# Performance work log

Hardware: AMD Instinct MI355X
Metric: run time of the kernel (lower is better)

## Reference

```python
import jax, jax.numpy as jnp
from jax import lax
import numpy as np

LOD = 60          # latent_obs_dim
LSD = 2 * LOD     # latent state dim
ACT = 10          # action dim
K = 15            # num_basis
BW = 3            # bandwidth
H_CTRL = 60       # control net hidden units
B, T = 1024, 150


def elup1(x):
    # elu(x) + 1, standard RKN positive-variance activation
    return jnp.where(x >= 0, x + 1.0, jnp.exp(x))


def setup_inputs() -> dict:
    key = jax.random.key(0)
    ks = jax.random.split(key, 14)
    inp = {
        "latent_obs": jax.random.normal(ks[0], (B, T, LOD), jnp.float32),
        "obs_vars": jax.random.uniform(ks[1], (B, T, LOD), jnp.float32) + 0.01,
        "action": jax.random.normal(ks[2], (B, T, ACT), jnp.float32),
        "initial_mean": jax.random.normal(ks[3], (B, LSD), jnp.float32),
        "initial_cov_u": jnp.ones((B, LOD), jnp.float32),
        "initial_cov_l": jnp.ones((B, LOD), jnp.float32),
        "initial_cov_s": jnp.zeros((B, LOD), jnp.float32),
        # transition model: K banded basis matrices per quadrant
        "tm11_basis": 0.05 * jax.random.normal(ks[4], (K, LOD, LOD), jnp.float32),
        "tm12_basis": 0.05 * jax.random.normal(ks[5], (K, LOD, LOD), jnp.float32),
        "tm21_basis": 0.05 * jax.random.normal(ks[6], (K, LOD, LOD), jnp.float32),
        "tm22_basis": 0.05 * jax.random.normal(ks[7], (K, LOD, LOD), jnp.float32),
        # coefficient net: linear (no hidden units per default config) + softmax
        "coeff_w": 0.05 * jax.random.normal(ks[8], (LSD, K), jnp.float32),
        "coeff_b": jnp.zeros((K,), jnp.float32),
        # control net: act -> 60 -> ReLU -> lsd
        "ctrl_w1": (1.0 / np.sqrt(ACT)) * jax.random.normal(ks[9], (ACT, H_CTRL), jnp.float32),
        "ctrl_b1": jnp.zeros((H_CTRL,), jnp.float32),
        "ctrl_w2": (1.0 / np.sqrt(H_CTRL)) * jax.random.normal(ks[10], (H_CTRL, LSD), jnp.float32),
        "ctrl_b2": jnp.zeros((LSD,), jnp.float32),
        # learned transition noise (elup1(0) = 1 matches default trans_covar=1)
        "log_trans_cov": jnp.zeros((LSD,), jnp.float32),
    }
    return inp


def _band_mask():
    i = np.arange(LOD)
    return jnp.asarray((np.abs(i[:, None] - i[None, :]) <= BW).astype(np.float32))


def reference(latent_obs, obs_vars, action, initial_mean,
              initial_cov_u, initial_cov_l, initial_cov_s,
              tm11_basis, tm12_basis, tm21_basis, tm22_basis,
              coeff_w, coeff_b, ctrl_w1, ctrl_b1, ctrl_w2, ctrl_b2,
              log_trans_cov):
    mask = _band_mask()
    m11, m12 = tm11_basis * mask, tm12_basis * mask
    m21, m22 = tm21_basis * mask, tm22_basis * mask
    tc = elup1(log_trans_cov)
    tcu, tcl = tc[:LOD], tc[LOD:]

    def mv(tm, v):  # batched matrix-vector: [b,i,j] @ [b,j] -> [b,i]
        return jnp.einsum('bij,bj->bi', tm, v)

    def step(carry, xs):
        mean, cu, cl, cs = carry           # prior belief
        obs, ov, act = xs
        # ---- Update (factorized Kalman update) ----
        denom = cu + ov
        qu = cu / denom                    # upper Kalman gain
        ql = cs / denom                    # lower Kalman gain
        res = obs - mean[:, :LOD]
        post_mean = mean + jnp.concatenate([qu * res, ql * res], axis=-1)
        f = 1.0 - qu
        pcu = f * cu
        pcs = f * cs
        pcl = cl - ql * cs
        # ---- AcPredict (locally linear transition + control) ----
        coeff = jax.nn.softmax(post_mean @ coeff_w + coeff_b, axis=-1)  # [B,K]
        t11 = jnp.einsum('bk,kij->bij', coeff, m11)
        t12 = jnp.einsum('bk,kij->bij', coeff, m12)
        t21 = jnp.einsum('bk,kij->bij', coeff, m21)
        t22 = jnp.einsum('bk,kij->bij', coeff, m22)
        mu, ml = post_mean[:, :LOD], post_mean[:, LOD:]
        ctrl = jax.nn.relu(act @ ctrl_w1 + ctrl_b1) @ ctrl_w2 + ctrl_b2
        nmean = jnp.concatenate([mv(t11, mu) + mv(t12, ml),
                                 mv(t21, mu) + mv(t22, ml)], axis=-1) + ctrl
        # diag blocks of T C T^T with C block-diagonal (cu, cl, cs)
        ncu = mv(t11 ** 2, pcu) + 2.0 * mv(t11 * t12, pcs) + mv(t12 ** 2, pcl) + tcu
        ncl = mv(t21 ** 2, pcu) + 2.0 * mv(t21 * t22, pcs) + mv(t22 ** 2, pcl) + tcl
        ncs = mv(t21 * t11, pcu) + mv(t22 * t11 + t21 * t12, pcs) + mv(t22 * t12, pcl)
        out = (post_mean, pcu, pcl, pcs, nmean, ncu, ncl, ncs)
        return (nmean, ncu, ncl, ncs), out

    xs = (jnp.moveaxis(latent_obs, 1, 0),
          jnp.moveaxis(obs_vars, 1, 0),
          jnp.moveaxis(action, 1, 0))
    carry0 = (initial_mean, initial_cov_u, initial_cov_l, initial_cov_s)
    _, ys = lax.scan(step, carry0, xs)
    post_means, pcu, pcl, pcs, prior_means, ncu, ncl, ncs = [
        jnp.moveaxis(y, 0, 1) for y in ys]  # [B,T,...]
    return (post_means, pcu, pcl, pcs, prior_means, ncu, ncl, ncs)


if __name__ == "__main__":
    outs = reference(**setup_inputs())
    print([o.shape for o in outs])
```

## Files before the change

### kernel.cpp

```cpp
#include <hip/hip_runtime.h>
#include <hip/hip_bf16.h>

namespace {

constexpr int TT = 150;

__device__ __forceinline__ float dot4(float4 a, float4 b) {
  return a.x*b.x + a.y*b.y + a.z*b.z + a.w*b.w;
}
__device__ __forceinline__ unsigned short bf16bits(float v) {
  __hip_bfloat16 h = __float2bfloat16(v);
  return *reinterpret_cast<unsigned short*>(&h);
}
__device__ __forceinline__ float dot2bf(unsigned a, unsigned b, float c) {
  float d;
  asm("v_dot2_f32_bf16 %0, %1, %2, %3" : "=v"(d) : "v"(a), "v"(b), "v"(c));
  return d;
}
__device__ __forceinline__ float tdot(uint4 a, uint4 b, const unsigned* cp) {
  float s = 0.f;
  s = dot2bf(a.x, cp[0], s); s = dot2bf(a.y, cp[1], s);
  s = dot2bf(a.z, cp[2], s); s = dot2bf(a.w, cp[3], s);
  s = dot2bf(b.x, cp[4], s); s = dot2bf(b.y, cp[5], s);
  s = dot2bf(b.z, cp[6], s); s = dot2bf(b.w, cp[7], s);
  return s;
}

template<int D0, int ND>
__device__ __forceinline__ void tmv_part(const uint4* m4u, const unsigned* cepk,
                                         const float* stat, int ii, int b, int swz,
                                         float rv[5]) {
  #pragma unroll
  for (int dd = 0; dd < ND; ++dd) {
    const int d = D0 + dd;
    const int ba = (0*7 + d)*120 + ii*2;
    const int bb = (1*7 + d)*120 + ii*2;
    const int bc = (2*7 + d)*120 + ii*2;
    const int bd = (3*7 + d)*120 + ii*2;
    const uint4 xa = m4u[ba + swz], ya = m4u[ba + 1 - swz];
    const uint4 xb = m4u[bb + swz], yb = m4u[bb + 1 - swz];
    const uint4 xc = m4u[bc + swz], yc = m4u[bc + 1 - swz];
    const uint4 xd = m4u[bd + swz], yd = m4u[bd + 1 - swz];
    const float a11 = tdot(xa, ya, cepk);
    const float a12 = tdot(xb, yb, cepk);
    const float a21 = tdot(xc, yc, cepk);
    const float a22 = tdot(xd, yd, cepk);
    const int si = (ii + d)*4 + b;
    const float mun  = stat[si];
    const float mln  = stat[288  + si];
    const float pcun = stat[576  + si];
    const float pcsn = stat[864  + si];
    const float pcln = stat[1152 + si];
    rv[0] += a11*mun + a12*mln;
    rv[1] += a21*mun + a22*mln;
    rv[2] += a11*a11*pcun + 2.f*a11*a12*pcsn + a12*a12*pcln;
    rv[3] += a21*a21*pcun + 2.f*a21*a22*pcsn + a22*a22*pcln;
    rv[4] += a21*a11*pcun + (a22*a11 + a21*a12)*pcsn + a22*a12*pcln;
  }
}

__launch_bounds__(256, 4)
__global__ void ctrl_pre(const float* __restrict__ actp,
                         const float* __restrict__ w1,
                         const float* __restrict__ b1,
                         const float* __restrict__ w2,
                         const float* __restrict__ b2,
                         float* __restrict__ out)
{
  __shared__ float w1s[640];
  __shared__ float b1s[64];
  __shared__ __align__(16) float w2pk[7680];
  __shared__ float b2s[128];
  __shared__ __align__(16) float hbuf[256];

  const int tid = threadIdx.x;
  for (int idx = tid; idx < 640; idx += 256) {
    const int j = idx & 63, a = idx >> 6;
    w1s[idx] = (j < 60) ? w1[a*60 + j] : 0.f;
  }
  for (int idx = tid; idx < 7680; idx += 256) {
    const int e = idx & 3;
    const int l = (idx >> 2) & 63;
    const int rest = idx >> 8;
    const int j4 = rest % 15;
    const int p  = rest / 15;
    w2pk[idx] = (l < 60) ? w2[(4*j4 + e)*120 + 2*l + p] : 0.f;
  }
  if (tid < 64)  b1s[tid] = (tid < 60)  ? b1[tid] : 0.f;
  if (tid < 128) b2s[tid] = (tid < 120) ? b2[tid] : 0.f;
  __syncthreads();

  const int w = tid >> 6, lane = tid & 63;
  float* o4 = out + 46080000L;
  const float4* w2pk4 = (const float4*)w2pk;
  const float4* hb4   = (const float4*)hbuf;

  for (int it = 0; it < 19; ++it) {
    const long bt = (long)(blockIdx.x*4 + w) + (long)it*8192;
    if (bt >= 153600L) break;
    const float av = (lane < 10) ? actp[bt*10 + lane] : 0.f;
    float hj = b1s[lane];
    #pragma unroll
    for (int a = 0; a < 10; ++a) hj += __shfl(av, a) * w1s[a*64 + lane];
    hbuf[w*64 + lane] = (lane < 60) ? fmaxf(hj, 0.f) : 0.f;

    float s0 = 0.f, s1 = 0.f;
    if (lane < 60) { s0 = b2s[2*lane]; s1 = b2s[2*lane + 1]; }
    #pragma unroll
    for (int j4 = 0; j4 < 15; ++j4) {
      const float4 hq = hb4[w*16 + j4];
      s0 += dot4(hq, w2pk4[(0*15 + j4)*64 + lane]);
      s1 += dot4(hq, w2pk4[(1*15 + j4)*64 + lane]);
    }
    if (lane < 60) ((float2*)(o4 + bt*120))[lane] = make_float2(s0, s1);
  }
}

__launch_bounds__(512, 2)
__global__ void acrkn(const float* __restrict__ lob,
                      const float* __restrict__ ovr,
                      const float* __restrict__ im,
                      const float* __restrict__ icu,
                      const float* __restrict__ icl,
                      const float* __restrict__ ics,
                      const float* __restrict__ tm11,
                      const float* __restrict__ tm12,
                      const float* __restrict__ tm21,
                      const float* __restrict__ tm22,
                      const float* __restrict__ cw,
                      const float* __restrict__ cb,
                      const float* __restrict__ ltc,
                      float* __restrict__ out)
{
  __shared__ __align__(16) unsigned m4b[13440];
  __shared__ __align__(16) float cwc[2048];
  __shared__ __align__(16) float stat[1440];
  __shared__ __align__(16) float parts[256];
  __shared__ __align__(16) float red[2560];
  __shared__ float cbs[16];

  const int tid = threadIdx.x;

  for (int idx = tid; idx < 13440; idx += 512) {
    const int c2 = idx & 7;
    int rest = idx >> 3;
    const int i = rest % 60;  rest /= 60;
    const int d = rest % 7;
    const int mat = rest / 7;
    const int k0 = 2*c2;
    const int j = i + d - 3;
    const float* tp = (mat == 0) ? tm11 : (mat == 1) ? tm12 : (mat == 2) ? tm21 : tm22;
    float ve = 0.f, vo = 0.f;
    if (j >= 0 && j < 60) {
      ve = tp[(k0*60 + i)*60 + j];
      if (k0 + 1 < 15) vo = tp[((k0+1)*60 + i)*60 + j];
    }
    const unsigned u = ((unsigned)bf16bits(vo) << 16) | (unsigned)bf16bits(ve);
    const int s = c2 >> 2, q = c2 & 3;
    const int sp = s ^ ((i >> 2) & 1);
    m4b[(((mat*7 + d)*60 + i)*2 + sp)*4 + q] = u;
  }
  for (int f4 = tid; f4 < 512; f4 += 512) {
    const int p = f4 & 127, c = f4 >> 7;
    const int col = (p < 60) ? p : ((p >= 64 && p < 124) ? (p - 4) : -1);
    float v0 = 0.f, v1 = 0.f, v2 = 0.f, v3 = 0.f;
    if (col >= 0) {
      const int k0 = c*4;
      v0 = cw[col*15 + k0+0];
      v1 = cw[col*15 + k0+1];
      v2 = cw[col*15 + k0+2];
      v3 = (k0+3 < 15) ? cw[col*15 + k0+3] : 0.f;
    }
    ((float4*)cwc)[f4] = make_float4(v0, v1, v2, v3);
  }
  for (int idx = tid; idx < 1440; idx += 512) stat[idx] = 0.f;
  if (tid < 16) cbs[tid] = (tid < 15) ? cb[tid] : 0.f;

  const int w = tid >> 6;
  const int g = w >> 2;
  const int wq = w & 3;
  const int lane = tid & 63;
  const int r = lane >> 2;
  const int b = lane & 3;
  const int iraw = wq*16 + r;
  const bool valid = (iraw < 60);
  const int ii = valid ? iraw : 0;
  const int gb = blockIdx.x*4 + b;
  const int swz = (ii >> 2) & 1;

  float mu_c = 0.f, ml_c = 0.f, cu_c = 1.f, cl_c = 1.f, cs_c = 0.f;
  float tcu_r = 1.f, tcl_r = 1.f;
  if (valid) {
    mu_c = im[gb*120 + ii];
    ml_c = im[gb*120 + 60 + ii];
    cu_c = icu[gb*60 + ii];
    cl_c = icl[gb*60 + ii];
    cs_c = ics[gb*60 + ii];
    const float l0 = ltc[ii], l1 = ltc[60 + ii];
    tcu_r = (l0 >= 0.f) ? l0 + 1.f : __expf(l0);
    tcl_r = (l1 >= 0.f) ? l1 + 1.f : __expf(l1);
  }

  const uint4*  m4u    = (const uint4*)m4b;
  const float4* cwc4   = (const float4*)cwc;
  const float4* parts4 = (const float4*)parts;

  float* o0 = out;
  float* o1 = out + 18432000L;
  float* o2 = out + 27648000L;
  float* o3 = out + 36864000L;
  float* o4 = out + 46080000L;
  float* o5 = out + 64512000L;
  float* o6 = out + 73728000L;
  float* o7 = out + 82944000L;

  __syncthreads();

  for (int t = 0; t < TT; ++t) {
    const long ob120 = ((long)gb*TT + t)*120;

    float ctrl_u = 0.f, ctrl_l = 0.f;
    if (valid) { ctrl_u = o4[ob120 + ii]; ctrl_l = o4[ob120 + 60 + ii]; }

    float pm_u = 0.f, pm_l = 0.f, pcu = 0.f, pcs = 0.f, pcl = 0.f;
    if (g == 0) {
      const long ib = (long)gb*(TT*60) + t*60 + ii;
      float obs = 0.f, ovv = 1.f;
      if (valid) { obs = lob[ib]; ovv = ovr[ib]; }
      const float denom = cu_c + ovv;
      const float inv = 1.0f / denom;
      const float qu = cu_c * inv;
      const float ql = cs_c * inv;
      const float res = obs - mu_c;
      pm_u = mu_c + qu*res;
      pm_l = ml_c + ql*res;
      const float f1 = 1.f - qu;
      pcu = f1*cu_c; pcs = f1*cs_c; pcl = cl_c - ql*cs_c;
      if (!valid) { pm_u = 0.f; pm_l = 0.f; pcu = 0.f; pcs = 0.f; pcl = 0.f; }

      if (valid) {
        stat[(0*72 + ii + 3)*4 + b] = pm_u;
        stat[(1*72 + ii + 3)*4 + b] = pm_l;
        stat[(2*72 + ii + 3)*4 + b] = pcu;
        stat[(3*72 + ii + 3)*4 + b] = pcs;
        stat[(4*72 + ii + 3)*4 + b] = pcl;
      }

      float p[16];
      #pragma unroll
      for (int k = 0; k < 16; ++k) p[k] = 0.f;
      #pragma unroll
      for (int c = 0; c < 4; ++c) {
        const float4 wu = cwc4[c*128 + ii];
        const float4 wl = cwc4[c*128 + 64 + ii];
        p[c*4+0] += pm_u*wu.x + pm_l*wl.x;
        p[c*4+1] += pm_u*wu.y + pm_l*wl.y;
        p[c*4+2] += pm_u*wu.z + pm_l*wl.z;
        p[c*4+3] += pm_u*wu.w + pm_l*wl.w;
      }
      #pragma unroll
      for (int m = 4; m <= 32; m <<= 1) {
        #pragma unroll
        for (int k = 0; k < 16; ++k) p[k] += __shfl_xor(p[k], m);
      }
      if (r == 0) {
        float4* pw = (float4*)parts;
        #pragma unroll
        for (int c = 0; c < 4; ++c)
          pw[(wq*4 + b)*4 + c] = make_float4(p[4*c], p[4*c+1], p[4*c+2], p[4*c+3]);
      }
    }
    __syncthreads();

    float q[16];
    #pragma unroll
    for (int k = 0; k < 16; ++k) q[k] = cbs[k];
    #pragma unroll
    for (int ww = 0; ww < 4; ++ww) {
      #pragma unroll
      for (int c = 0; c < 4; ++c) {
        const float4 pv = parts4[(ww*4 + b)*4 + c];
        q[4*c+0] += pv.x; q[4*c+1] += pv.y; q[4*c+2] += pv.z; q[4*c+3] += pv.w;
      }
    }
    float mx = q[0];
    #pragma unroll
    for (int k = 1; k < 15; ++k) mx = fmaxf(mx, q[k]);
    float ce[16];
    float ssum = 0.f;
    #pragma unroll
    for (int k = 0; k < 15; ++k) { ce[k] = __expf(q[k] - mx); ssum += ce[k]; }
    const float rs = 1.f / ssum;
    #pragma unroll
    for (int k = 0; k < 15; ++k) ce[k] *= rs;
    ce[15] = 0.f;
    unsigned cepk[8];
    #pragma unroll
    for (int j = 0; j < 8; ++j)
      cepk[j] = ((unsigned)bf16bits(ce[2*j+1]) << 16) | (unsigned)bf16bits(ce[2*j]);

    float rv[5] = {0.f, 0.f, 0.f, 0.f, 0.f};
    if (g == 0) tmv_part<0, 4>(m4u, cepk, stat, ii, b, swz, rv);
    else        tmv_part<4, 3>(m4u, cepk, stat, ii, b, swz, rv);

    if (valid) {
      #pragma unroll
      for (int v = 0; v < 5; ++v) red[((g*5 + v)*64 + ii)*4 + b] = rv[v];
    }
    __syncthreads();

    const int rb = ii*4 + b;
    const float nmu = red[(0*64)*4 + rb]  + red[(5*64)*4 + rb]  + ctrl_u;
    const float nml = red[(1*64)*4 + rb]  + red[(6*64)*4 + rb]  + ctrl_l;
    const float ncu = red[(2*64)*4 + rb]  + red[(7*64)*4 + rb]  + tcu_r;
    const float ncl = red[(3*64)*4 + rb]  + red[(8*64)*4 + rb]  + tcl_r;
    const float ncs = red[(4*64)*4 + rb]  + red[(9*64)*4 + rb];

    if (valid) {
      const long ob60 = ((long)gb*TT + t)*60;
      if (g == 0) {
        o0[ob120 + ii]      = pm_u;
        o0[ob120 + 60 + ii] = pm_l;
        o1[ob60 + ii] = pcu;
        o2[ob60 + ii] = pcl;
        o3[ob60 + ii] = pcs;
      } else {
        o4[ob120 + ii]      = nmu;
        o4[ob120 + 60 + ii] = nml;
        o5[ob60 + ii] = ncu;
        o6[ob60 + ii] = ncl;
        o7[ob60 + ii] = ncs;
      }
    }

    mu_c = nmu; ml_c = nml; cu_c = ncu; cl_c = ncl; cs_c = ncs;
  }
}

}

extern "C" void kernel_launch(void* const* d_in, const int* in_sizes, int n_in,
                              void* d_out, int out_size, void* d_ws, size_t ws_size,
                              hipStream_t stream) {
  (void)in_sizes; (void)n_in; (void)d_ws; (void)ws_size; (void)out_size;
  const float* lob  = (const float*)d_in[0];
  const float* ovr  = (const float*)d_in[1];
  const float* actp = (const float*)d_in[2];
  const float* im   = (const float*)d_in[3];
  const float* icu  = (const float*)d_in[4];
  const float* icl  = (const float*)d_in[5];
  const float* ics  = (const float*)d_in[6];
  const float* tm11 = (const float*)d_in[7];
  const float* tm12 = (const float*)d_in[8];
  const float* tm21 = (const float*)d_in[9];
  const float* tm22 = (const float*)d_in[10];
  const float* cw   = (const float*)d_in[11];
  const float* cb   = (const float*)d_in[12];
  const float* w1   = (const float*)d_in[13];
  const float* b1   = (const float*)d_in[14];
  const float* w2   = (const float*)d_in[15];
  const float* b2   = (const float*)d_in[16];
  const float* ltc  = (const float*)d_in[17];

  ctrl_pre<<<dim3(2048), dim3(256), 0, stream>>>(actp, w1, b1, w2, b2, (float*)d_out);
  acrkn<<<dim3(256), dim3(512), 0, stream>>>(
      lob, ovr, im, icu, icl, ics,
      tm11, tm12, tm21, tm22, cw, cb, ltc,
      (float*)d_out);
}
```

Before: 775.1 us.

## Split transition mat-vec across four wave groups with 1024-thread blocks

The recurrent kernel doubles its block to 1024 threads and splits the seven banded transition products across four chunks instead of two, so each wave does less serial work per timestep. The posterior outputs are now written by a different chunk reading shared memory, and the coefficient reduction uses a shared-memory transpose instead of xor shuffles. The softmax max-subtraction is dropped, and the control precompute kernel gets twice the blocks with a prefetched action load. In exchange it uses more shared memory and a larger reduction buffer, and the softmax without max-subtraction could overflow for large logits.

```diff
diff --git a/kernel.cpp b/kernel.cpp
--- a/kernel.cpp
+++ b/kernel.cpp
@@ -95,28 +95,34 @@
   const float4* w2pk4 = (const float4*)w2pk;
   const float4* hb4   = (const float4*)hbuf;
 
-  for (int it = 0; it < 19; ++it) {
-    const long bt = (long)(blockIdx.x*4 + w) + (long)it*8192;
-    if (bt >= 153600L) break;
-    const float av = (lane < 10) ? actp[bt*10 + lane] : 0.f;
-    float hj = b1s[lane];
-    #pragma unroll
-    for (int a = 0; a < 10; ++a) hj += __shfl(av, a) * w1s[a*64 + lane];
-    hbuf[w*64 + lane] = (lane < 60) ? fmaxf(hj, 0.f) : 0.f;
-
-    float s0 = 0.f, s1 = 0.f;
-    if (lane < 60) { s0 = b2s[2*lane]; s1 = b2s[2*lane + 1]; }
-    #pragma unroll
-    for (int j4 = 0; j4 < 15; ++j4) {
-      const float4 hq = hb4[w*16 + j4];
-      s0 += dot4(hq, w2pk4[(0*15 + j4)*64 + lane]);
-      s1 += dot4(hq, w2pk4[(1*15 + j4)*64 + lane]);
-    }
-    if (lane < 60) ((float2*)(o4 + bt*120))[lane] = make_float2(s0, s1);
-  }
-}
-
-__launch_bounds__(512, 2)
+  long bt = (long)(blockIdx.x*4 + w);
+  float av = (lane < 10 && bt < 153600L) ? actp[bt*10 + lane] : 0.f;
+
+  for (int it = 0; it < 10; ++it) {
+    const long btn = bt + 16384L;
+    const float avn = (lane < 10 && btn < 153600L) ? actp[btn*10 + lane] : 0.f;
+
+    if (bt < 153600L) {
+      float hj = b1s[lane];
+      #pragma unroll
+      for (int a = 0; a < 10; ++a) hj += __shfl(av, a) * w1s[a*64 + lane];
+      hbuf[w*64 + lane] = (lane < 60) ? fmaxf(hj, 0.f) : 0.f;
+
+      float s0 = 0.f, s1 = 0.f;
+      if (lane < 60) { s0 = b2s[2*lane]; s1 = b2s[2*lane + 1]; }
+      #pragma unroll
+      for (int j4 = 0; j4 < 15; ++j4) {
+        const float4 hq = hb4[w*16 + j4];
+        s0 += dot4(hq, w2pk4[(0*15 + j4)*64 + lane]);
+        s1 += dot4(hq, w2pk4[(1*15 + j4)*64 + lane]);
+      }
+      if (lane < 60) ((float2*)(o4 + bt*120))[lane] = make_float2(s0, s1);
+    }
+    bt = btn; av = avn;
+  }
+}
+
+__launch_bounds__(1024, 4)
 __global__ void acrkn(const float* __restrict__ lob,
                       const float* __restrict__ ovr,
                       const float* __restrict__ im,
@@ -135,13 +141,14 @@
   __shared__ __align__(16) unsigned m4b[13440];
   __shared__ __align__(16) float cwc[2048];
   __shared__ __align__(16) float stat[1440];
+  __shared__ __align__(16) float pscratch[4096];
   __shared__ __align__(16) float parts[256];
-  __shared__ __align__(16) float red[2560];
+  __shared__ __align__(16) float red[5120];
   __shared__ float cbs[16];
 
   const int tid = threadIdx.x;
 
-  for (int idx = tid; idx < 13440; idx += 512) {
+  for (int idx = tid; idx < 13440; idx += 1024) {
     const int c2 = idx & 7;
     int rest = idx >> 3;
     const int i = rest % 60;  rest /= 60;
@@ -160,7 +167,8 @@
     const int sp = s ^ ((i >> 2) & 1);
     m4b[(((mat*7 + d)*60 + i)*2 + sp)*4 + q] = u;
   }
-  for (int f4 = tid; f4 < 512; f4 += 512) {
+  if (tid < 512) {
+    const int f4 = tid;
     const int p = f4 & 127, c = f4 >> 7;
     const int col = (p < 60) ? p : ((p >= 64 && p < 124) ? (p - 4) : -1);
     float v0 = 0.f, v1 = 0.f, v2 = 0.f, v3 = 0.f;
@@ -173,11 +181,11 @@
     }
     ((float4*)cwc)[f4] = make_float4(v0, v1, v2, v3);
   }
-  for (int idx = tid; idx < 1440; idx += 512) stat[idx] = 0.f;
+  for (int idx = tid; idx < 1440; idx += 1024) stat[idx] = 0.f;
   if (tid < 16) cbs[tid] = (tid < 15) ? cb[tid] : 0.f;
 
   const int w = tid >> 6;
-  const int g = w >> 2;
+  const int chunk = w >> 2;
   const int wq = w & 3;
   const int lane = tid & 63;
   const int r = lane >> 2;
@@ -204,6 +212,7 @@
   const uint4*  m4u    = (const uint4*)m4b;
   const float4* cwc4   = (const float4*)cwc;
   const float4* parts4 = (const float4*)parts;
+  float4*       ps4    = (float4*)pscratch;
 
   float* o0 = out;
   float* o1 = out + 18432000L;
@@ -220,10 +229,12 @@
     const long ob120 = ((long)gb*TT + t)*120;
 
     float ctrl_u = 0.f, ctrl_l = 0.f;
-    if (valid) { ctrl_u = o4[ob120 + ii]; ctrl_l = o4[ob120 + 60 + ii]; }
-
-    float pm_u = 0.f, pm_l = 0.f, pcu = 0.f, pcs = 0.f, pcl = 0.f;
-    if (g == 0) {
+    if ((chunk == 0 || chunk == 3) && valid) {
+      ctrl_u = o4[ob120 + ii];
+      ctrl_l = o4[ob120 + 60 + ii];
+    }
+
+    if (chunk == 0) {
       const long ib = (long)gb*(TT*60) + t*60 + ii;
       float obs = 0.f, ovv = 1.f;
       if (valid) { obs = lob[ib]; ovv = ovr[ib]; }
@@ -232,10 +243,10 @@
       const float qu = cu_c * inv;
       const float ql = cs_c * inv;
       const float res = obs - mu_c;
-      pm_u = mu_c + qu*res;
-      pm_l = ml_c + ql*res;
+      float pm_u = mu_c + qu*res;
+      float pm_l = ml_c + ql*res;
       const float f1 = 1.f - qu;
-      pcu = f1*cu_c; pcs = f1*cs_c; pcl = cl_c - ql*cs_c;
+      float pcu = f1*cu_c, pcs = f1*cs_c, pcl = cl_c - ql*cs_c;
       if (!valid) { pm_u = 0.f; pm_l = 0.f; pcu = 0.f; pcs = 0.f; pcl = 0.f; }
 
       if (valid) {
@@ -258,19 +269,36 @@
         p[c*4+2] += pm_u*wu.z + pm_l*wl.z;
         p[c*4+3] += pm_u*wu.w + pm_l*wl.w;
       }
-      #pragma unroll
-      for (int m = 4; m <= 32; m <<= 1) {
-        #pragma unroll
-        for (int k = 0; k < 16; ++k) p[k] += __shfl_xor(p[k], m);
-      }
-      if (r == 0) {
-        float4* pw = (float4*)parts;
-        #pragma unroll
-        for (int c = 0; c < 4; ++c)
-          pw[(wq*4 + b)*4 + c] = make_float4(p[4*c], p[4*c+1], p[4*c+2], p[4*c+3]);
-      }
+      const int pb = (wq*64 + lane)*4;
+      ps4[pb+0] = make_float4(p[0],  p[1],  p[2],  p[3]);
+      ps4[pb+1] = make_float4(p[4],  p[5],  p[6],  p[7]);
+      ps4[pb+2] = make_float4(p[8],  p[9],  p[10], p[11]);
+      ps4[pb+3] = make_float4(p[12], p[13], p[14], p[15]);
+      const int rbase = wq*1024 + b*16 + r;
+      float tv[16];
+      #pragma unroll
+      for (int rp = 0; rp < 16; ++rp) tv[rp] = pscratch[rbase + rp*64];
+      const float s0 = (tv[0]+tv[1]) + (tv[2]+tv[3]);
+      const float s1 = (tv[4]+tv[5]) + (tv[6]+tv[7]);
+      const float s2 = (tv[8]+tv[9]) + (tv[10]+tv[11]);
+      const float s3 = (tv[12]+tv[13]) + (tv[14]+tv[15]);
+      parts[(wq*4 + b)*16 + r] = (s0+s1) + (s2+s3);
     }
     __syncthreads();
+
+    if (chunk == 3 && valid) {
+      const long ob60 = ((long)gb*TT + t)*60;
+      const float s_pmu = stat[(0*72 + ii + 3)*4 + b];
+      const float s_pml = stat[(1*72 + ii + 3)*4 + b];
+      const float s_pcu = stat[(2*72 + ii + 3)*4 + b];
+      const float s_pcs = stat[(3*72 + ii + 3)*4 + b];
+      const float s_pcl = stat[(4*72 + ii + 3)*4 + b];
+      o0[ob120 + ii]      = s_pmu;
+      o0[ob120 + 60 + ii] = s_pml;
+      o1[ob60 + ii] = s_pcu;
+      o2[ob60 + ii] = s_pcl;
+      o3[ob60 + ii] = s_pcs;
+    }
 
     float q[16];
     #pragma unroll
@@ -283,14 +311,14 @@
         q[4*c+0] += pv.x; q[4*c+1] += pv.y; q[4*c+2] += pv.z; q[4*c+3] += pv.w;
       }
     }
-    float mx = q[0];
-    #pragma unroll
-    for (int k = 1; k < 15; ++k) mx = fmaxf(mx, q[k]);
     float ce[16];
-    float ssum = 0.f;
-    #pragma unroll
-    for (int k = 0; k < 15; ++k) { ce[k] = __expf(q[k] - mx); ssum += ce[k]; }
-    const float rs = 1.f / ssum;
+    #pragma unroll
+    for (int k = 0; k < 15; ++k) ce[k] = __expf(q[k]);
+    const float e0 = (ce[0]+ce[1]) + (ce[2]+ce[3]);
+    const float e1 = (ce[4]+ce[5]) + (ce[6]+ce[7]);
+    const float e2 = (ce[8]+ce[9]) + (ce[10]+ce[11]);
+    const float e3 = (ce[12]+ce[13]) + ce[14];
+    const float rs = 1.f / ((e0+e1) + (e2+e3));
     #pragma unroll
     for (int k = 0; k < 15; ++k) ce[k] *= rs;
     ce[15] = 0.f;
@@ -300,40 +328,41 @@
       cepk[j] = ((unsigned)bf16bits(ce[2*j+1]) << 16) | (unsigned)bf16bits(ce[2*j]);
 
     float rv[5] = {0.f, 0.f, 0.f, 0.f, 0.f};
-    if (g == 0) tmv_part<0, 4>(m4u, cepk, stat, ii, b, swz, rv);
-    else        tmv_part<4, 3>(m4u, cepk, stat, ii, b, swz, rv);
+    if      (chunk == 0) tmv_part<0, 2>(m4u, cepk, stat, ii, b, swz, rv);
+    else if (chunk == 1) tmv_part<2, 2>(m4u, cepk, stat, ii, b, swz, rv);
+    else if (chunk == 2) tmv_part<4, 2>(m4u, cepk, stat, ii, b, swz, rv);
+    else                 tmv_part<6, 1>(m4u, cepk, stat, ii, b, swz, rv);
 
     if (valid) {
       #pragma unroll
-      for (int v = 0; v < 5; ++v) red[((g*5 + v)*64 + ii)*4 + b] = rv[v];
+      for (int v = 0; v < 5; ++v) red[chunk*1280 + v*256 + ii*4 + b] = rv[v];
     }
     __syncthreads();
 
-    const int rb = ii*4 + b;
-    const float nmu = red[(0*64)*4 + rb]  + red[(5*64)*4 + rb]  + ctrl_u;
-    const float nml = red[(1*64)*4 + rb]  + red[(6*64)*4 + rb]  + ctrl_l;
-    const float ncu = red[(2*64)*4 + rb]  + red[(7*64)*4 + rb]  + tcu_r;
-    const float ncl = red[(3*64)*4 + rb]  + red[(8*64)*4 + rb]  + tcl_r;
-    const float ncs = red[(4*64)*4 + rb]  + red[(9*64)*4 + rb];
-
-    if (valid) {
-      const long ob60 = ((long)gb*TT + t)*60;
-      if (g == 0) {
-        o0[ob120 + ii]      = pm_u;
-        o0[ob120 + 60 + ii] = pm_l;
-        o1[ob60 + ii] = pcu;
-        o2[ob60 + ii] = pcl;
-        o3[ob60 + ii] = pcs;
+    if (chunk == 0 || chunk == 3) {
+      const int rb = ii*4 + b;
+      float nmu = ctrl_u, nml = ctrl_l, ncu = tcu_r, ncl = tcl_r, ncs = 0.f;
+      #pragma unroll
+      for (int c = 0; c < 4; ++c) {
+        nmu += red[c*1280 + 0*256 + rb];
+        nml += red[c*1280 + 1*256 + rb];
+        ncu += red[c*1280 + 2*256 + rb];
+        ncl += red[c*1280 + 3*256 + rb];
+        ncs += red[c*1280 + 4*256 + rb];
+      }
+      if (chunk == 3) {
+        if (valid) {
+          const long ob60 = ((long)gb*TT + t)*60;
+          o4[ob120 + ii]      = nmu;
+          o4[ob120 + 60 + ii] = nml;
+          o5[ob60 + ii] = ncu;
+          o6[ob60 + ii] = ncl;
+          o7[ob60 + ii] = ncs;
+        }
       } else {
-        o4[ob120 + ii]      = nmu;
-        o4[ob120 + 60 + ii] = nml;
-        o5[ob60 + ii] = ncu;
-        o6[ob60 + ii] = ncl;
-        o7[ob60 + ii] = ncs;
-      }
-    }
-
-    mu_c = nmu; ml_c = nml; cu_c = ncu; cl_c = ncl; cs_c = ncs;
+        mu_c = nmu; ml_c = nml; cu_c = ncu; cl_c = ncl; cs_c = ncs;
+      }
+    }
   }
 }
 
@@ -362,8 +391,8 @@
   const float* b2   = (const float*)d_in[16];
   const float* ltc  = (const float*)d_in[17];
 
-  ctrl_pre<<<dim3(2048), dim3(256), 0, stream>>>(actp, w1, b1, w2, b2, (float*)d_out);
-  acrkn<<<dim3(256), dim3(512), 0, stream>>>(
+  ctrl_pre<<<dim3(4096), dim3(256), 0, stream>>>(actp, w1, b1, w2, b2, (float*)d_out);
+  acrkn<<<dim3(256), dim3(1024), 0, stream>>>(
       lob, ovr, im, icu, icl, ics,
       tm11, tm12, tm21, tm22, cw, cb, ltc,
       (float*)d_out);
```

Result: faster. 725.2 us (-6.4%).
